# Optimization experiments

Hardware: AMD Instinct MI355X
Metric: run time of the kernel (lower is better)

The kernel has to match this reference:

```python
import jax, jax.numpy as jnp
import numpy as np

N = 50000      # nodes
E = 400000     # edges (before self-loops)
IN = 128
HID = 64
HEADS = 8
OUT = 3
NEG_SLOPE = 0.2
EPS = 1e-6


def setup_inputs() -> dict:
    key = jax.random.key(0)
    ks = jax.random.split(key, 32)
    def nrm(k, shape, s=0.05):
        return jax.random.normal(k, shape, dtype=jnp.float32) * s
    inp = {}
    inp['x'] = nrm(ks[0], (N, IN), 1.0)
    inp['edge_index'] = jax.random.randint(ks[1], (2, E), 0, N)
    inp['res_W'] = nrm(ks[2], (OUT, IN))
    inp['res_b'] = jnp.zeros((OUT,), jnp.float32)
    # (in, out, heads, concat) per GAT layer
    dims = [(IN, HID, HEADS, True), (HID * HEADS, HID, HEADS, True),
            (HID * HEADS, HID, HEADS, True), (HID * HEADS, OUT, 1, False)]
    j = 3
    for i, (ci, co, h, cc) in enumerate(dims):
        inp['ln_g%d' % i] = jnp.ones((ci,), jnp.float32)
        inp['ln_b%d' % i] = jnp.zeros((ci,), jnp.float32)
        inp['W%d' % i] = nrm(ks[j], (h * co, ci)); j += 1
        inp['asr%d' % i] = nrm(ks[j], (h, co)); j += 1
        inp['adt%d' % i] = nrm(ks[j], (h, co)); j += 1
        inp['b%d' % i] = jnp.zeros((h * co if cc else co,), jnp.float32)
    return inp


def layer_norm(x, g, b):
    mu = x.mean(-1, keepdims=True)
    var = ((x - mu) ** 2).mean(-1, keepdims=True)
    return (x - mu) / jnp.sqrt(var + EPS) * g + b


def gat_conv(x, src, dst, W, a_src, a_dst, bias, heads, co, concat):
    n = x.shape[0]
    h = (x @ W.T).reshape(n, heads, co)                    # [N,H,C]
    al_src = jnp.sum(h * a_src, axis=-1)                   # [N,H]
    al_dst = jnp.sum(h * a_dst, axis=-1)                   # [N,H]
    e = jax.nn.leaky_relu(al_src[src] + al_dst[dst], NEG_SLOPE)  # [E',H]
    # segment softmax over incoming edges of each destination node
    m = jax.ops.segment_max(e, dst, num_segments=n)
    e = jnp.exp(e - m[dst])
    s = jax.ops.segment_sum(e, dst, num_segments=n)
    alpha = e / s[dst]                                     # [E',H]
    msg = h[src] * alpha[..., None]                        # [E',H,C]
    out = jax.ops.segment_sum(msg, dst, num_segments=n)    # [N,H,C]
    out = out.reshape(n, heads * co) if concat else out.mean(axis=1)
    return out + bias


def reference(x, edge_index, res_W, res_b,
              ln_g0, ln_b0, W0, asr0, adt0, b0,
              ln_g1, ln_b1, W1, asr1, adt1, b1,
              ln_g2, ln_b2, W2, asr2, adt2, b2,
              ln_g3, ln_b3, W3, asr3, adt3, b3):
    n = x.shape[0]
    loops = jnp.arange(n)
    src = jnp.concatenate([edge_index[0], loops])          # add self-loops (PyG default)
    dst = jnp.concatenate([edge_index[1], loops])
    residual = x @ res_W.T + res_b
    layers = [(ln_g0, ln_b0, W0, asr0, adt0, b0, HEADS, HID, True),
              (ln_g1, ln_b1, W1, asr1, adt1, b1, HEADS, HID, True),
              (ln_g2, ln_b2, W2, asr2, adt2, b2, HEADS, HID, True),
              (ln_g3, ln_b3, W3, asr3, adt3, b3, 1, OUT, False)]
    h = x
    num_layers = len(layers)
    for i, (g, bb, W, a_s, a_d, bi, hd, co, cc) in enumerate(layers):
        x_res = h
        h = layer_norm(h, g, bb)
        h = gat_conv(h, src, dst, W, a_s, a_d, bi, hd, co, cc)
        if i < num_layers - 1:
            h = jax.nn.gelu(h, approximate=False)
            if h.shape == x_res.shape:
                h = h + x_res
    return h + residual
```

## Files before the change

kernel.cpp:

```cpp
#include <hip/hip_runtime.h>
#include <math.h>

#define NN 50000
#define MPAD 50048
#define EE 400000
#define NE 450000
#define IN_F 128
#define NEG_SLOPE 0.2f
#define EPSV 1e-6f

typedef unsigned short bf16u;
typedef short bf8_t __attribute__((ext_vector_type(8)));
typedef float f32x4 __attribute__((ext_vector_type(4)));

__device__ __forceinline__ float bf2f(unsigned int u) {
    return __uint_as_float(u << 16);
}
__device__ __forceinline__ bf16u f2bf(float f) {
    unsigned int u = __float_as_uint(f);
    unsigned int r = (u + 0x7FFFu + ((u >> 16) & 1u)) >> 16;
    return (bf16u)r;
}
__device__ __forceinline__ float gelu_f(float v) {
    return 0.5f * v * (1.0f + erff(v * 0.70710678118654752f));
}

__device__ __forceinline__ void gload_lds16(const void* g, void* l) {
    __builtin_amdgcn_global_load_lds(
        (__attribute__((address_space(1))) void*)(g),
        (__attribute__((address_space(3))) void*)(l), 16, 0, 0);
}

__global__ void k_zero_i32(int* p, int n) {
    int i = blockIdx.x * 256 + threadIdx.x;
    if (i < n) p[i] = 0;
}

__global__ void k_deg(const int* __restrict__ ei, int* __restrict__ deg) {
    int i = blockIdx.x * 256 + threadIdx.x;
    if (i >= NE) return;
    int d = (i < EE) ? ei[EE + i] : (i - EE);
    atomicAdd(&deg[d], 1);
}

__global__ __launch_bounds__(256) void k_scan1(const int* __restrict__ deg,
                                               int* __restrict__ incl,
                                               int* __restrict__ bsums, int n) {
    __shared__ int sm[1024];
    int base = blockIdx.x * 1024;
    for (int i = threadIdx.x; i < 1024; i += 256)
        sm[i] = (base + i < n) ? deg[base + i] : 0;
    __syncthreads();
    for (int off = 1; off < 1024; off <<= 1) {
        int v[4];
#pragma unroll
        for (int j = 0; j < 4; j++) {
            int i = threadIdx.x + 256 * j;
            v[j] = (i >= off) ? sm[i - off] : 0;
        }
        __syncthreads();
#pragma unroll
        for (int j = 0; j < 4; j++) {
            int i = threadIdx.x + 256 * j;
            sm[i] += v[j];
        }
        __syncthreads();
    }
    for (int i = threadIdx.x; i < 1024; i += 256)
        if (base + i < n) incl[base + i] = sm[i];
    if (threadIdx.x == 0) bsums[blockIdx.x] = sm[1023];
}

__global__ void k_scan2(int* bsums, int nb) {
    if (threadIdx.x == 0 && blockIdx.x == 0) {
        int run = 0;
        for (int i = 0; i < nb; i++) { int v = bsums[i]; bsums[i] = run; run += v; }
    }
}

__global__ void k_scan3(const int* __restrict__ deg, int* __restrict__ rowptr,
                        int* __restrict__ cursor, const int* __restrict__ bsums,
                        int n, int ne) {
    int i = blockIdx.x * 256 + threadIdx.x;
    if (i < n) {
        int excl = rowptr[i] + bsums[i >> 10] - deg[i];
        rowptr[i] = excl;
        cursor[i] = excl;
    }
    if (i == n) rowptr[n] = ne;
}

__global__ void k_scatter(const int* __restrict__ ei, int* __restrict__ cursor,
                          int* __restrict__ col) {
    int i = blockIdx.x * 256 + threadIdx.x;
    if (i >= NE) return;
    int s, d;
    if (i < EE) { s = ei[i]; d = ei[EE + i]; }
    else        { s = i - EE; d = i - EE; }
    int p = atomicAdd(&cursor[d], 1);
    col[p] = s;
}

__global__ void k_cast(const float* __restrict__ x, bf16u* __restrict__ h, int total) {
    int i = blockIdx.x * 256 + threadIdx.x;
    if (i < total) h[i] = f2bf(x[i]);
}

__global__ __launch_bounds__(256) void k_castln(const float* __restrict__ x,
                                                bf16u* __restrict__ h,
                                                float* __restrict__ stats, int n) {
    int row = (blockIdx.x * 256 + threadIdx.x) >> 6;
    int lane = threadIdx.x & 63;
    if (row >= n) return;
    float2 v = *(const float2*)(x + (size_t)row * 128 + lane * 2);
    unsigned int pk = (unsigned int)f2bf(v.x) | ((unsigned int)f2bf(v.y) << 16);
    *(unsigned int*)(h + (size_t)row * 128 + lane * 2) = pk;
    float s = v.x + v.y, s2 = v.x * v.x + v.y * v.y;
#pragma unroll
    for (int off = 32; off; off >>= 1) {
        s  += __shfl_xor(s, off);
        s2 += __shfl_xor(s2, off);
    }
    if (lane == 0) {
        float mu = s * (1.0f / 128.0f);
        float var = s2 * (1.0f / 128.0f) - mu * mu;
        stats[row * 2 + 0] = mu;
        stats[row * 2 + 1] = rsqrtf(var + EPSV);
    }
}

__global__ __launch_bounds__(256) void k_residual(const float* __restrict__ x,
                                                  const float* __restrict__ rw,
                                                  const float* __restrict__ rb,
                                                  float* __restrict__ res) {
    int gw = (blockIdx.x * 256 + threadIdx.x) >> 6;
    int lane = threadIdx.x & 63;
    if (gw >= NN) return;
    float a0 = 0.f, a1 = 0.f, a2 = 0.f;
    for (int k = lane; k < IN_F; k += 64) {
        float xv = x[(size_t)gw * IN_F + k];
        a0 += xv * rw[0 * IN_F + k];
        a1 += xv * rw[1 * IN_F + k];
        a2 += xv * rw[2 * IN_F + k];
    }
#pragma unroll
    for (int off = 32; off; off >>= 1) {
        a0 += __shfl_down(a0, off);
        a1 += __shfl_down(a1, off);
        a2 += __shfl_down(a2, off);
    }
    if (lane == 0) {
        res[gw * 3 + 0] = a0 + rb[0];
        res[gw * 3 + 1] = a1 + rb[1];
        res[gw * 3 + 2] = a2 + rb[2];
    }
}

#define BM 128
#define BN 128
#define BKK 32
__global__ __launch_bounds__(256) void k_gemm_mfma(const bf16u* __restrict__ H,
                                                   const float* __restrict__ stats,
                                                   const float* __restrict__ g,
                                                   const float* __restrict__ bbias,
                                                   const bf16u* __restrict__ Wb,
                                                   bf16u* __restrict__ C,
                                                   int Mreal, int ci, int K) {
    __shared__ __align__(16) bf16u As[BM * BKK];
    __shared__ __align__(16) bf16u Bs[BN * BKK];
    const int tid = threadIdx.x;
    const int w = tid >> 6, lane = tid & 63;
    const int row0 = blockIdx.x * BM, col0 = blockIdx.y * BN;
    const int wr = (w >> 1) * 64, wc = (w & 1) * 64;

    const int srow = w * 32 + (lane >> 2);
    const int scol = (lane & 3) * 8;
    const bf16u* gA = H + (size_t)(row0 + srow) * ci + scol;
    const bf16u* gB = Wb + (size_t)(col0 + srow) * ci + scol;
    const float mu1 = stats[(row0 + srow) * 2 + 0];
    const float rs1 = stats[(row0 + srow) * 2 + 1];
    const float mu2 = stats[(row0 + srow + 16) * 2 + 0];
    const float rs2 = stats[(row0 + srow + 16) * 2 + 1];
    bf16u* lA1 = &As[(size_t)srow * BKK + scol];
    bf16u* lA2 = &As[(size_t)(srow + 16) * BKK + scol];
    void* lB1 = &Bs[(size_t)(w * 32) * BKK];
    void* lB2 = &Bs[(size_t)(w * 32 + 16) * BKK];

    f32x4 acc[4][4] = {};

    const int fr = lane & 15;
    const int fk = (lane >> 4) * 8;

    for (int k0 = 0; k0 < ci; k0 += BKK) {
        uint4 ra1 = *(const uint4*)(gA + k0);
        uint4 ra2 = *(const uint4*)(gA + (size_t)16 * ci + k0);
        float4 g0 = *(const float4*)(g + k0 + scol);
        float4 g1 = *(const float4*)(g + k0 + scol + 4);
        float4 b0 = *(const float4*)(bbias + k0 + scol);
        float4 b1 = *(const float4*)(bbias + k0 + scol + 4);
        float gg[8] = {g0.x, g0.y, g0.z, g0.w, g1.x, g1.y, g1.z, g1.w};
        float bb[8] = {b0.x, b0.y, b0.z, b0.w, b1.x, b1.y, b1.z, b1.w};
        unsigned int u1[4] = {ra1.x, ra1.y, ra1.z, ra1.w};
        unsigned int u2[4] = {ra2.x, ra2.y, ra2.z, ra2.w};
        uint4 p1, p2;
        {
            unsigned int po[4], qo[4];
#pragma unroll
            for (int j = 0; j < 4; j++) {
                float va = (bf2f(u1[j] & 0xFFFFu) - mu1) * rs1;
                float vb = (bf2f(u1[j] >> 16)     - mu1) * rs1;
                float oa = fmaf(va, gg[2 * j], bb[2 * j]);
                float ob = fmaf(vb, gg[2 * j + 1], bb[2 * j + 1]);
                po[j] = (unsigned int)f2bf(oa) | ((unsigned int)f2bf(ob) << 16);
                float vc = (bf2f(u2[j] & 0xFFFFu) - mu2) * rs2;
                float vd = (bf2f(u2[j] >> 16)     - mu2) * rs2;
                float oc = fmaf(vc, gg[2 * j], bb[2 * j]);
                float od = fmaf(vd, gg[2 * j + 1], bb[2 * j + 1]);
                qo[j] = (unsigned int)f2bf(oc) | ((unsigned int)f2bf(od) << 16);
            }
            p1 = make_uint4(po[0], po[1], po[2], po[3]);
            p2 = make_uint4(qo[0], qo[1], qo[2], qo[3]);
        }

        __syncthreads();
        *(uint4*)lA1 = p1;
        *(uint4*)lA2 = p2;
        gload_lds16(gB + k0, lB1);
        gload_lds16(gB + (size_t)16 * ci + k0, lB2);
        __syncthreads();

        bf8_t af[4], bf[4];
#pragma unroll
        for (int m = 0; m < 4; m++)
            af[m] = *(const bf8_t*)&As[(size_t)(wr + m * 16 + fr) * BKK + fk];
#pragma unroll
        for (int n = 0; n < 4; n++)
            bf[n] = *(const bf8_t*)&Bs[(size_t)(wc + n * 16 + fr) * BKK + fk];
#pragma unroll
        for (int m = 0; m < 4; m++)
#pragma unroll
            for (int n = 0; n < 4; n++)
                acc[m][n] = __builtin_amdgcn_mfma_f32_16x16x32_bf16(af[m], bf[n], acc[m][n], 0, 0, 0);
    }

    const int fc = lane & 15;
    const int fq = (lane >> 4) * 4;
#pragma unroll
    for (int m = 0; m < 4; m++) {
#pragma unroll
        for (int r = 0; r < 4; r++) {
            int row = row0 + wr + m * 16 + fq + r;
            if (row >= Mreal) continue;
#pragma unroll
            for (int n = 0; n < 4; n++) {
                int col = col0 + wc + n * 16 + fc;
                C[(size_t)row * K + col] = f2bf(acc[m][n][r]);
            }
        }
    }
}

__global__ __launch_bounds__(256) void k_al2(const bf16u* __restrict__ hlin,
                                             const float* __restrict__ asr,
                                             const float* __restrict__ adt,
                                             float* __restrict__ alsrc,
                                             float* __restrict__ aldst, int n) {
    int row = (blockIdx.x * 256 + threadIdx.x) >> 6;
    int lane = threadIdx.x & 63;
    if (row >= n) return;
    int h = lane >> 3, c0 = (lane & 7) * 8;
    uint4 u = *(const uint4*)(hlin + (size_t)row * 512 + lane * 8);
    const float* as = asr + h * 64 + c0;
    const float* ad = adt + h * 64 + c0;
    float4 s0 = *(const float4*)as, s1 = *(const float4*)(as + 4);
    float4 d0 = *(const float4*)ad, d1 = *(const float4*)(ad + 4);
    float v0 = bf2f(u.x & 0xFFFFu), v1 = bf2f(u.x >> 16);
    float v2 = bf2f(u.y & 0xFFFFu), v3 = bf2f(u.y >> 16);
    float v4 = bf2f(u.z & 0xFFFFu), v5 = bf2f(u.z >> 16);
    float v6 = bf2f(u.w & 0xFFFFu), v7 = bf2f(u.w >> 16);
    float ss = v0 * s0.x + v1 * s0.y + v2 * s0.z + v3 * s0.w
             + v4 * s1.x + v5 * s1.y + v6 * s1.z + v7 * s1.w;
    float dd = v0 * d0.x + v1 * d0.y + v2 * d0.z + v3 * d0.w
             + v4 * d1.x + v5 * d1.y + v6 * d1.z + v7 * d1.w;
#pragma unroll
    for (int off = 4; off; off >>= 1) {
        ss += __shfl_xor(ss, off);
        dd += __shfl_xor(dd, off);
    }
    if ((lane & 7) == 0) {
        alsrc[row * 8 + h] = ss;
        aldst[row * 8 + h] = dd;
    }
}

__global__ __launch_bounds__(256) void k_lin3(const bf16u* __restrict__ h,
                                              const float* __restrict__ stats,
                                              const float* __restrict__ g,
                                              const float* __restrict__ bb,
                                              const float* __restrict__ W,
                                              const float* __restrict__ a_s,
                                              const float* __restrict__ a_d,
                                              bf16u* __restrict__ hlin3,
                                              float* __restrict__ alsrc,
                                              float* __restrict__ aldst, int n) {
    int row = (blockIdx.x * 256 + threadIdx.x) >> 6;
    int lane = threadIdx.x & 63;
    if (row >= n) return;
    float mu = stats[row * 2 + 0], rs = stats[row * 2 + 1];
    uint4 r = *(const uint4*)(h + (size_t)row * 512 + lane * 8);
    float4 g0 = *(const float4*)(g + lane * 8);
    float4 g1 = *(const float4*)(g + lane * 8 + 4);
    float4 b0 = *(const float4*)(bb + lane * 8);
    float4 b1 = *(const float4*)(bb + lane * 8 + 4);
    float gg[8] = {g0.x, g0.y, g0.z, g0.w, g1.x, g1.y, g1.z, g1.w};
    float bv[8] = {b0.x, b0.y, b0.z, b0.w, b1.x, b1.y, b1.z, b1.w};
    unsigned int u[4] = {r.x, r.y, r.z, r.w};
    float ln[8];
#pragma unroll
    for (int j = 0; j < 4; j++) {
        ln[2 * j]     = fmaf((bf2f(u[j] & 0xFFFFu) - mu) * rs, gg[2 * j], bv[2 * j]);
        ln[2 * j + 1] = fmaf((bf2f(u[j] >> 16)     - mu) * rs, gg[2 * j + 1], bv[2 * j + 1]);
    }
    float a0 = 0.f, a1 = 0.f, a2 = 0.f;
#pragma unroll
    for (int j = 0; j < 8; j++) {
        int k = lane * 8 + j;
        a0 += ln[j] * W[k];
        a1 += ln[j] * W[512 + k];
        a2 += ln[j] * W[1024 + k];
    }
#pragma unroll
    for (int off = 32; off; off >>= 1) {
        a0 += __shfl_down(a0, off);
        a1 += __shfl_down(a1, off);
        a2 += __shfl_down(a2, off);
    }
    if (lane == 0) {
        hlin3[row * 3 + 0] = f2bf(a0);
        hlin3[row * 3 + 1] = f2bf(a1);
        hlin3[row * 3 + 2] = f2bf(a2);
        alsrc[row] = a0 * a_s[0] + a1 * a_s[1] + a2 * a_s[2];
        aldst[row] = a0 * a_d[0] + a1 * a_d[1] + a2 * a_d[2];
    }
}

__global__ __launch_bounds__(256) void k_aggN(const bf16u* __restrict__ hlin,
                                              const float* __restrict__ alsrc,
                                              const float* __restrict__ aldst,
                                              const int* __restrict__ rowptr,
                                              const int* __restrict__ col,
                                              const float* __restrict__ bias,
                                              bf16u* __restrict__ hio,
                                              float* __restrict__ stats,
                                              int n, int dores) {
    __shared__ float alds[4][8][66];
    int wv = threadIdx.x >> 6;
    int node = (blockIdx.x * 256 + threadIdx.x) >> 6;
    int lane = threadIdx.x & 63;
    if (node >= n) return;
    int beg = rowptr[node], end = rowptr[node + 1];
    int deg = end - beg;

    const float4* dv = (const float4*)(aldst + node * 8);
    float4 da = dv[0], db = dv[1];
    float ad[8] = {da.x, da.y, da.z, da.w, db.x, db.y, db.z, db.w};

    float s = 0.f, s2 = 0.f;

    if (deg <= 64) {
        int srcreg = 0;
        float raw[8];
#pragma unroll
        for (int h = 0; h < 8; h++) raw[h] = -INFINITY;
        if (lane < deg) {
            srcreg = col[beg + lane];
            const float4* sv = (const float4*)(alsrc + srcreg * 8);
            float4 sa = sv[0], sb = sv[1];
            float sl[8] = {sa.x, sa.y, sa.z, sa.w, sb.x, sb.y, sb.z, sb.w};
#pragma unroll
            for (int h = 0; h < 8; h++) {
                float v = sl[h] + ad[h];
                raw[h] = (v >= 0.f) ? v : NEG_SLOPE * v;
            }
        }
        float m[8];
#pragma unroll
        for (int h = 0; h < 8; h++) m[h] = raw[h];
#pragma unroll
        for (int off = 32; off; off >>= 1)
#pragma unroll
            for (int h = 0; h < 8; h++) m[h] = fmaxf(m[h], __shfl_xor(m[h], off));
        float ex[8], sm[8];
#pragma unroll
        for (int h = 0; h < 8; h++) {
            ex[h] = (lane < deg) ? __expf(raw[h] - m[h]) : 0.f;
            sm[h] = ex[h];
        }
#pragma unroll
        for (int off = 32; off; off >>= 1)
#pragma unroll
            for (int h = 0; h < 8; h++) sm[h] += __shfl_xor(sm[h], off);
#pragma unroll
        for (int h = 0; h < 8; h++)
            alds[wv][h][lane] = ex[h] * (1.0f / sm[h]);
        asm volatile("s_waitcnt lgkmcnt(0)" ::: "memory");

        int hl = lane >> 3;
        const float* myal = &alds[wv][hl][0];
        float acc[8] = {};
        for (int e = 0; e < deg; e++) {
            float alpha = myal[e];
            int src = __shfl(srcreg, e);
            uint4 u = *(const uint4*)(hlin + ((size_t)src << 9) + (lane << 3));
            acc[0] = fmaf(alpha, bf2f(u.x & 0xFFFFu), acc[0]);
            acc[1] = fmaf(alpha, bf2f(u.x >> 16),     acc[1]);
            acc[2] = fmaf(alpha, bf2f(u.y & 0xFFFFu), acc[2]);
            acc[3] = fmaf(alpha, bf2f(u.y >> 16),     acc[3]);
            acc[4] = fmaf(alpha, bf2f(u.z & 0xFFFFu), acc[4]);
            acc[5] = fmaf(alpha, bf2f(u.z >> 16),     acc[5]);
            acc[6] = fmaf(alpha, bf2f(u.w & 0xFFFFu), acc[6]);
            acc[7] = fmaf(alpha, bf2f(u.w >> 16),     acc[7]);
        }

        size_t idx = (size_t)node * 512 + lane * 8;
        float4 b0 = *(const float4*)(bias + lane * 8);
        float4 b1 = *(const float4*)(bias + lane * 8 + 4);
        float bb[8] = {b0.x, b0.y, b0.z, b0.w, b1.x, b1.y, b1.z, b1.w};
        float fin[8];
#pragma unroll
        for (int j = 0; j < 8; j++) fin[j] = gelu_f(acc[j] + bb[j]);
        if (dores) {
            uint4 up = *(const uint4*)(hio + idx);
            fin[0] += bf2f(up.x & 0xFFFFu); fin[1] += bf2f(up.x >> 16);
            fin[2] += bf2f(up.y & 0xFFFFu); fin[3] += bf2f(up.y >> 16);
            fin[4] += bf2f(up.z & 0xFFFFu); fin[5] += bf2f(up.z >> 16);
            fin[6] += bf2f(up.w & 0xFFFFu); fin[7] += bf2f(up.w >> 16);
        }
        uint4 pk;
        pk.x = (unsigned int)f2bf(fin[0]) | ((unsigned int)f2bf(fin[1]) << 16);
        pk.y = (unsigned int)f2bf(fin[2]) | ((unsigned int)f2bf(fin[3]) << 16);
        pk.z = (unsigned int)f2bf(fin[4]) | ((unsigned int)f2bf(fin[5]) << 16);
        pk.w = (unsigned int)f2bf(fin[6]) | ((unsigned int)f2bf(fin[7]) << 16);
        *(uint4*)(hio + idx) = pk;
#pragma unroll
        for (int j = 0; j < 8; j++) { s += fin[j]; s2 += fin[j] * fin[j]; }
    } else {
        for (int h = 0; h < 8; h++) {
            float adh = ad[h];
            float m = -INFINITY;
            for (int e = beg + lane; e < end; e += 64) {
                float v = alsrc[col[e] * 8 + h] + adh;
                v = (v >= 0.f) ? v : NEG_SLOPE * v;
                m = fmaxf(m, v);
            }
#pragma unroll
            for (int off = 32; off; off >>= 1) m = fmaxf(m, __shfl_xor(m, off));
            float sum = 0.f;
            for (int e = beg + lane; e < end; e += 64) {
                float v = alsrc[col[e] * 8 + h] + adh;
                v = (v >= 0.f) ? v : NEG_SLOPE * v;
                sum += __expf(v - m);
            }
#pragma unroll
            for (int off = 32; off; off >>= 1) sum += __shfl_xor(sum, off);
            float inv = 1.0f / sum;
            float acc = 0.f;
            for (int e = beg; e < end; e++) {
                int src = col[e];
                float v = alsrc[src * 8 + h] + adh;
                v = (v >= 0.f) ? v : NEG_SLOPE * v;
                float alpha = __expf(v - m) * inv;
                acc = fmaf(alpha, bf2f(hlin[((size_t)src << 9) + h * 64 + lane]), acc);
            }
            float fin = gelu_f(acc + bias[h * 64 + lane]);
            size_t idx = (size_t)node * 512 + h * 64 + lane;
            if (dores) fin += bf2f(hio[idx]);
            hio[idx] = f2bf(fin);
            s += fin; s2 += fin * fin;
        }
    }

#pragma unroll
    for (int off = 32; off; off >>= 1) {
        s  += __shfl_xor(s, off);
        s2 += __shfl_xor(s2, off);
    }
    if (lane == 0) {
        float mu = s * (1.0f / 512.0f);
        float var = s2 * (1.0f / 512.0f) - mu * mu;
        stats[node * 2 + 0] = mu;
        stats[node * 2 + 1] = rsqrtf(var + EPSV);
    }
}

__global__ __launch_bounds__(256) void k_aggF(const bf16u* __restrict__ hlin,
                                              const float* __restrict__ alsrc,
                                              const float* __restrict__ aldst,
                                              const int* __restrict__ rowptr,
                                              const int* __restrict__ col,
                                              const float* __restrict__ bias,
                                              float* __restrict__ outf,
                                              const float* __restrict__ resid, int n) {
    int node = (blockIdx.x * 256 + threadIdx.x) >> 6;
    int lane = threadIdx.x & 63;
    if (node >= n) return;
    int beg = rowptr[node], end = rowptr[node + 1];
    float adh = aldst[node];

    float m = -INFINITY;
    for (int e = beg + lane; e < end; e += 64) {
        float v = alsrc[col[e]] + adh;
        v = (v >= 0.f) ? v : NEG_SLOPE * v;
        m = fmaxf(m, v);
    }
#pragma unroll
    for (int off = 32; off; off >>= 1) m = fmaxf(m, __shfl_xor(m, off));

    float sum = 0.f;
    for (int e = beg + lane; e < end; e += 64) {
        float v = alsrc[col[e]] + adh;
        v = (v >= 0.f) ? v : NEG_SLOPE * v;
        sum += __expf(v - m);
    }
#pragma unroll
    for (int off = 32; off; off >>= 1) sum += __shfl_xor(sum, off);
    float inv = 1.0f / sum;

    float acc = 0.f;
    for (int e = beg; e < end; e++) {
        int src = col[e];
        float v = alsrc[src] + adh;
        v = (v >= 0.f) ? v : NEG_SLOPE * v;
        float alpha = __expf(v - m) * inv;
        if (lane < 3) acc += alpha * bf2f(hlin[(size_t)src * 3 + lane]);
    }
    if (lane < 3)
        outf[node * 3 + lane] = acc + bias[lane] + resid[node * 3 + lane];
}

extern "C" void kernel_launch(void* const* d_in, const int* in_sizes, int n_in,
                              void* d_out, int out_size, void* d_ws, size_t ws_size,
                              hipStream_t stream) {
    const float* x    = (const float*)d_in[0];
    const int*   ei   = (const int*)d_in[1];
    const float* resW = (const float*)d_in[2];
    const float* resb = (const float*)d_in[3];
    const float *lng[4], *lnb[4], *Wm[4], *asr[4], *adt[4], *bias[4];
    int idx = 4;
    for (int i = 0; i < 4; i++) {
        lng[i]  = (const float*)d_in[idx++];
        lnb[i]  = (const float*)d_in[idx++];
        Wm[i]   = (const float*)d_in[idx++];
        asr[i]  = (const float*)d_in[idx++];
        adt[i]  = (const float*)d_in[idx++];
        bias[i] = (const float*)d_in[idx++];
    }

    char* base = (char*)d_ws;
    size_t off = 0;
    auto alloc = [&](size_t bytes) {
        void* p = base + off;
        off += (bytes + 255) & ~(size_t)255;
        return p;
    };
    bf16u* hbuf  = (bf16u*)alloc((size_t)MPAD * 512 * 2);
    bf16u* lbuf  = (bf16u*)alloc((size_t)MPAD * 512 * 2);
    bf16u* wb0   = (bf16u*)alloc((size_t)512 * 128 * 2);
    bf16u* wb1   = (bf16u*)alloc((size_t)512 * 512 * 2);
    bf16u* wb2   = (bf16u*)alloc((size_t)512 * 512 * 2);
    float* stats = (float*)alloc((size_t)MPAD * 2 * 4);
    float* alsrc = (float*)alloc((size_t)NN * 8 * 4);
    float* aldst = (float*)alloc((size_t)NN * 8 * 4);
    float* resid = (float*)alloc((size_t)NN * 3 * 4);
    int* rowptr  = (int*)alloc((size_t)(NN + 1) * 4);
    int* cursor  = (int*)alloc((size_t)NN * 4);
    int* deg     = (int*)alloc((size_t)NN * 4);
    int* colidx  = (int*)alloc((size_t)NE * 4);
    int* bsums   = (int*)alloc(256 * 4);
    if (off > ws_size) return;

    float* out = (float*)d_out;

    k_zero_i32<<<(NN + 255) / 256, 256, 0, stream>>>(deg, NN);
    k_deg<<<(NE + 255) / 256, 256, 0, stream>>>(ei, deg);
    int nb = (NN + 1023) / 1024;
    k_scan1<<<nb, 256, 0, stream>>>(deg, rowptr, bsums, NN);
    k_scan2<<<1, 64, 0, stream>>>(bsums, nb);
    k_scan3<<<(NN + 1 + 255) / 256, 256, 0, stream>>>(deg, rowptr, cursor, bsums, NN, NE);
    k_scatter<<<(NE + 255) / 256, 256, 0, stream>>>(ei, cursor, colidx);

    int rowBlocks = (NN * 64 + 255) / 256;
    k_residual<<<rowBlocks, 256, 0, stream>>>(x, resW, resb, resid);
    k_castln<<<rowBlocks, 256, 0, stream>>>(x, hbuf, stats, NN);
    k_cast<<<(512 * 128 + 255) / 256, 256, 0, stream>>>(Wm[0], wb0, 512 * 128);
    k_cast<<<(512 * 512 + 255) / 256, 256, 0, stream>>>(Wm[1], wb1, 512 * 512);
    k_cast<<<(512 * 512 + 255) / 256, 256, 0, stream>>>(Wm[2], wb2, 512 * 512);

    const bf16u* wb[3] = {wb0, wb1, wb2};
    const int ci_a[3] = {128, 512, 512};

    for (int i = 0; i < 3; i++) {
        int ci = ci_a[i];
        int dores = (i >= 1) ? 1 : 0;

        dim3 ggrid(MPAD / BM, 512 / BN);
        k_gemm_mfma<<<ggrid, 256, 0, stream>>>(hbuf, stats, lng[i], lnb[i], wb[i],
                                               lbuf, NN, ci, 512);

        k_al2<<<rowBlocks, 256, 0, stream>>>(lbuf, asr[i], adt[i], alsrc, aldst, NN);

        k_aggN<<<rowBlocks, 256, 0, stream>>>(lbuf, alsrc, aldst, rowptr, colidx,
                                              bias[i], hbuf, stats, NN, dores);
    }

    k_lin3<<<rowBlocks, 256, 0, stream>>>(hbuf, stats, lng[3], lnb[3], Wm[3],
                                          asr[3], adt[3], lbuf, alsrc, aldst, NN);
    k_aggF<<<rowBlocks, 256, 0, stream>>>(lbuf, alsrc, aldst, rowptr, colidx,
                                          bias[3], out, resid, NN);
}
```

Measured before the change: 704.5 us.

## Fuse attention logits into GEMM epilogue, merge residual into cast, rework aggregation

Computes the per-head attention logits (alsrc/aldst) in the MFMA GEMM epilogue from fp32 accumulators. This removes the separate k_al2 pass that re-read the bf16 projection. The residual projection is merged into the cast/LayerNorm-stats kernel, so x is read once. The aggregation kernel stores precomputed byte offsets next to alpha in LDS and unrolls the gather by two. The final layer uses a padded 4-wide hlin3 layout with a single-pass warp softmax for low-degree nodes. Logits now come from unrounded fp32 values instead of bf16, which slightly changes numerics, and the epilogue adds shuffle reductions.

New measurement: 670.1 us. 4.9% less time.

```diff
diff --git a/kernel.cpp b/kernel.cpp
--- a/kernel.cpp
+++ b/kernel.cpp
@@ -15,6 +15,9 @@
 
 __device__ __forceinline__ float bf2f(unsigned int u) {
     return __uint_as_float(u << 16);
+}
+__device__ __forceinline__ float bf2f_hi(unsigned int u) {
+    return __uint_as_float(u & 0xFFFF0000u);
 }
 __device__ __forceinline__ bf16u f2bf(float f) {
     unsigned int u = __float_as_uint(f);
@@ -106,53 +109,41 @@
     if (i < total) h[i] = f2bf(x[i]);
 }
 
-__global__ __launch_bounds__(256) void k_castln(const float* __restrict__ x,
-                                                bf16u* __restrict__ h,
-                                                float* __restrict__ stats, int n) {
+__global__ __launch_bounds__(256) void k_castres(const float* __restrict__ x,
+                                                 const float* __restrict__ rw,
+                                                 const float* __restrict__ rb,
+                                                 bf16u* __restrict__ h,
+                                                 float* __restrict__ stats,
+                                                 float* __restrict__ res, int n) {
     int row = (blockIdx.x * 256 + threadIdx.x) >> 6;
     int lane = threadIdx.x & 63;
     if (row >= n) return;
     float2 v = *(const float2*)(x + (size_t)row * 128 + lane * 2);
     unsigned int pk = (unsigned int)f2bf(v.x) | ((unsigned int)f2bf(v.y) << 16);
     *(unsigned int*)(h + (size_t)row * 128 + lane * 2) = pk;
+    float2 w0 = *(const float2*)(rw + 0 * 128 + lane * 2);
+    float2 w1 = *(const float2*)(rw + 1 * 128 + lane * 2);
+    float2 w2 = *(const float2*)(rw + 2 * 128 + lane * 2);
     float s = v.x + v.y, s2 = v.x * v.x + v.y * v.y;
+    float a0 = v.x * w0.x + v.y * w0.y;
+    float a1 = v.x * w1.x + v.y * w1.y;
+    float a2 = v.x * w2.x + v.y * w2.y;
 #pragma unroll
     for (int off = 32; off; off >>= 1) {
         s  += __shfl_xor(s, off);
         s2 += __shfl_xor(s2, off);
+        a0 += __shfl_xor(a0, off);
+        a1 += __shfl_xor(a1, off);
+        a2 += __shfl_xor(a2, off);
     }
     if (lane == 0) {
         float mu = s * (1.0f / 128.0f);
         float var = s2 * (1.0f / 128.0f) - mu * mu;
         stats[row * 2 + 0] = mu;
         stats[row * 2 + 1] = rsqrtf(var + EPSV);
-    }
-}
-
-__global__ __launch_bounds__(256) void k_residual(const float* __restrict__ x,
-                                                  const float* __restrict__ rw,
-                                                  const float* __restrict__ rb,
-                                                  float* __restrict__ res) {
-    int gw = (blockIdx.x * 256 + threadIdx.x) >> 6;
-    int lane = threadIdx.x & 63;
-    if (gw >= NN) return;
-    float a0 = 0.f, a1 = 0.f, a2 = 0.f;
-    for (int k = lane; k < IN_F; k += 64) {
-        float xv = x[(size_t)gw * IN_F + k];
-        a0 += xv * rw[0 * IN_F + k];
-        a1 += xv * rw[1 * IN_F + k];
-        a2 += xv * rw[2 * IN_F + k];
-    }
-#pragma unroll
-    for (int off = 32; off; off >>= 1) {
-        a0 += __shfl_down(a0, off);
-        a1 += __shfl_down(a1, off);
-        a2 += __shfl_down(a2, off);
-    }
-    if (lane == 0) {
-        res[gw * 3 + 0] = a0 + rb[0];
-        res[gw * 3 + 1] = a1 + rb[1];
-        res[gw * 3 + 2] = a2 + rb[2];
+        res[row * 3 + 0] = a0 + rb[0];
+        res[row * 3 + 1] = a1 + rb[1];
+        res[row * 3 + 2] = a2 + rb[2];
     }
 }
 
@@ -165,6 +156,10 @@
                                                    const float* __restrict__ bbias,
                                                    const bf16u* __restrict__ Wb,
                                                    bf16u* __restrict__ C,
+                                                   const float* __restrict__ asr,
+                                                   const float* __restrict__ adt,
+                                                   float* __restrict__ alsrc,
+                                                   float* __restrict__ aldst,
                                                    int Mreal, int ci, int K) {
     __shared__ __align__(16) bf16u As[BM * BKK];
     __shared__ __align__(16) bf16u Bs[BN * BKK];
@@ -208,12 +203,12 @@
 #pragma unroll
             for (int j = 0; j < 4; j++) {
                 float va = (bf2f(u1[j] & 0xFFFFu) - mu1) * rs1;
-                float vb = (bf2f(u1[j] >> 16)     - mu1) * rs1;
+                float vb = (bf2f_hi(u1[j])         - mu1) * rs1;
                 float oa = fmaf(va, gg[2 * j], bb[2 * j]);
                 float ob = fmaf(vb, gg[2 * j + 1], bb[2 * j + 1]);
                 po[j] = (unsigned int)f2bf(oa) | ((unsigned int)f2bf(ob) << 16);
                 float vc = (bf2f(u2[j] & 0xFFFFu) - mu2) * rs2;
-                float vd = (bf2f(u2[j] >> 16)     - mu2) * rs2;
+                float vd = (bf2f_hi(u2[j])         - mu2) * rs2;
                 float oc = fmaf(vc, gg[2 * j], bb[2 * j]);
                 float od = fmaf(vd, gg[2 * j + 1], bb[2 * j + 1]);
                 qo[j] = (unsigned int)f2bf(oc) | ((unsigned int)f2bf(od) << 16);
@@ -245,6 +240,7 @@
 
     const int fc = lane & 15;
     const int fq = (lane >> 4) * 4;
+
 #pragma unroll
     for (int m = 0; m < 4; m++) {
 #pragma unroll
@@ -258,38 +254,33 @@
             }
         }
     }
-}
-
-__global__ __launch_bounds__(256) void k_al2(const bf16u* __restrict__ hlin,
-                                             const float* __restrict__ asr,
-                                             const float* __restrict__ adt,
-                                             float* __restrict__ alsrc,
-                                             float* __restrict__ aldst, int n) {
-    int row = (blockIdx.x * 256 + threadIdx.x) >> 6;
-    int lane = threadIdx.x & 63;
-    if (row >= n) return;
-    int h = lane >> 3, c0 = (lane & 7) * 8;
-    uint4 u = *(const uint4*)(hlin + (size_t)row * 512 + lane * 8);
-    const float* as = asr + h * 64 + c0;
-    const float* ad = adt + h * 64 + c0;
-    float4 s0 = *(const float4*)as, s1 = *(const float4*)(as + 4);
-    float4 d0 = *(const float4*)ad, d1 = *(const float4*)(ad + 4);
-    float v0 = bf2f(u.x & 0xFFFFu), v1 = bf2f(u.x >> 16);
-    float v2 = bf2f(u.y & 0xFFFFu), v3 = bf2f(u.y >> 16);
-    float v4 = bf2f(u.z & 0xFFFFu), v5 = bf2f(u.z >> 16);
-    float v6 = bf2f(u.w & 0xFFFFu), v7 = bf2f(u.w >> 16);
-    float ss = v0 * s0.x + v1 * s0.y + v2 * s0.z + v3 * s0.w
-             + v4 * s1.x + v5 * s1.y + v6 * s1.z + v7 * s1.w;
-    float dd = v0 * d0.x + v1 * d0.y + v2 * d0.z + v3 * d0.w
-             + v4 * d1.x + v5 * d1.y + v6 * d1.z + v7 * d1.w;
-#pragma unroll
-    for (int off = 4; off; off >>= 1) {
-        ss += __shfl_xor(ss, off);
-        dd += __shfl_xor(dd, off);
-    }
-    if ((lane & 7) == 0) {
-        alsrc[row * 8 + h] = ss;
-        aldst[row * 8 + h] = dd;
+
+    const int head = blockIdx.y * 2 + (wc >> 6);
+    float av[4], dv[4];
+#pragma unroll
+    for (int n = 0; n < 4; n++) {
+        av[n] = asr[head * 64 + n * 16 + fc];
+        dv[n] = adt[head * 64 + n * 16 + fc];
+    }
+#pragma unroll
+    for (int m = 0; m < 4; m++) {
+#pragma unroll
+        for (int r = 0; r < 4; r++) {
+            float s1 = acc[m][0][r] * av[0] + acc[m][1][r] * av[1]
+                     + acc[m][2][r] * av[2] + acc[m][3][r] * av[3];
+            float s2 = acc[m][0][r] * dv[0] + acc[m][1][r] * dv[1]
+                     + acc[m][2][r] * dv[2] + acc[m][3][r] * dv[3];
+#pragma unroll
+            for (int o = 1; o < 16; o <<= 1) {
+                s1 += __shfl_xor(s1, o);
+                s2 += __shfl_xor(s2, o);
+            }
+            int row = row0 + wr + m * 16 + fq + r;
+            if (fc == 0 && row < Mreal) {
+                alsrc[row * 8 + head] = s1;
+                aldst[row * 8 + head] = s2;
+            }
+        }
     }
 }
 
@@ -319,7 +310,7 @@
 #pragma unroll
     for (int j = 0; j < 4; j++) {
         ln[2 * j]     = fmaf((bf2f(u[j] & 0xFFFFu) - mu) * rs, gg[2 * j], bv[2 * j]);
-        ln[2 * j + 1] = fmaf((bf2f(u[j] >> 16)     - mu) * rs, gg[2 * j + 1], bv[2 * j + 1]);
+        ln[2 * j + 1] = fmaf((bf2f_hi(u[j])         - mu) * rs, gg[2 * j + 1], bv[2 * j + 1]);
     }
     float a0 = 0.f, a1 = 0.f, a2 = 0.f;
 #pragma unroll
@@ -336,9 +327,9 @@
         a2 += __shfl_down(a2, off);
     }
     if (lane == 0) {
-        hlin3[row * 3 + 0] = f2bf(a0);
-        hlin3[row * 3 + 1] = f2bf(a1);
-        hlin3[row * 3 + 2] = f2bf(a2);
+        *(unsigned int*)(hlin3 + (size_t)row * 4) =
+            (unsigned int)f2bf(a0) | ((unsigned int)f2bf(a1) << 16);
+        *(unsigned int*)(hlin3 + (size_t)row * 4 + 2) = (unsigned int)f2bf(a2);
         alsrc[row] = a0 * a_s[0] + a1 * a_s[1] + a2 * a_s[2];
         aldst[row] = a0 * a_d[0] + a1 * a_d[1] + a2 * a_d[2];
     }
@@ -353,7 +344,7 @@
                                               bf16u* __restrict__ hio,
                                               float* __restrict__ stats,
                                               int n, int dores) {
-    __shared__ float alds[4][8][66];
+    __shared__ uint2 aldsU[4][8][66];
     int wv = threadIdx.x >> 6;
     int node = (blockIdx.x * 256 + threadIdx.x) >> 6;
     int lane = threadIdx.x & 63;
@@ -361,19 +352,20 @@
     int beg = rowptr[node], end = rowptr[node + 1];
     int deg = end - beg;
 
-    const float4* dv = (const float4*)(aldst + node * 8);
-    float4 da = dv[0], db = dv[1];
+    const float4* dvv = (const float4*)(aldst + node * 8);
+    float4 da = dvv[0], db = dvv[1];
     float ad[8] = {da.x, da.y, da.z, da.w, db.x, db.y, db.z, db.w};
 
     float s = 0.f, s2 = 0.f;
 
     if (deg <= 64) {
-        int srcreg = 0;
+        unsigned int offb = 0;
         float raw[8];
 #pragma unroll
         for (int h = 0; h < 8; h++) raw[h] = -INFINITY;
         if (lane < deg) {
-            srcreg = col[beg + lane];
+            int srcreg = col[beg + lane];
+            offb = (unsigned int)srcreg << 10;
             const float4* sv = (const float4*)(alsrc + srcreg * 8);
             float4 sa = sv[0], sb = sv[1];
             float sl[8] = {sa.x, sa.y, sa.z, sa.w, sb.x, sb.y, sb.z, sb.w};
@@ -401,25 +393,54 @@
 #pragma unroll
             for (int h = 0; h < 8; h++) sm[h] += __shfl_xor(sm[h], off);
 #pragma unroll
-        for (int h = 0; h < 8; h++)
-            alds[wv][h][lane] = ex[h] * (1.0f / sm[h]);
+        for (int h = 0; h < 8; h++) {
+            uint2 t;
+            t.x = __float_as_uint(ex[h] * (1.0f / sm[h]));
+            t.y = offb;
+            aldsU[wv][h][lane] = t;
+        }
         asm volatile("s_waitcnt lgkmcnt(0)" ::: "memory");
 
         int hl = lane >> 3;
-        const float* myal = &alds[wv][hl][0];
+        const uint2* myal = &aldsU[wv][hl][0];
+        const char* base2 = (const char*)hlin + (lane << 4);
         float acc[8] = {};
-        for (int e = 0; e < deg; e++) {
-            float alpha = myal[e];
-            int src = __shfl(srcreg, e);
-            uint4 u = *(const uint4*)(hlin + ((size_t)src << 9) + (lane << 3));
-            acc[0] = fmaf(alpha, bf2f(u.x & 0xFFFFu), acc[0]);
-            acc[1] = fmaf(alpha, bf2f(u.x >> 16),     acc[1]);
-            acc[2] = fmaf(alpha, bf2f(u.y & 0xFFFFu), acc[2]);
-            acc[3] = fmaf(alpha, bf2f(u.y >> 16),     acc[3]);
-            acc[4] = fmaf(alpha, bf2f(u.z & 0xFFFFu), acc[4]);
-            acc[5] = fmaf(alpha, bf2f(u.z >> 16),     acc[5]);
-            acc[6] = fmaf(alpha, bf2f(u.w & 0xFFFFu), acc[6]);
-            acc[7] = fmaf(alpha, bf2f(u.w >> 16),     acc[7]);
+        int e = 0;
+        for (; e + 2 <= deg; e += 2) {
+            uint2 t0 = myal[e];
+            uint2 t1 = myal[e + 1];
+            uint4 u0 = *(const uint4*)(base2 + t0.y);
+            uint4 u1 = *(const uint4*)(base2 + t1.y);
+            float a0 = __uint_as_float(t0.x), a1 = __uint_as_float(t1.x);
+            acc[0] = fmaf(a0, bf2f(u0.x & 0xFFFFu), acc[0]);
+            acc[1] = fmaf(a0, bf2f_hi(u0.x),        acc[1]);
+            acc[2] = fmaf(a0, bf2f(u0.y & 0xFFFFu), acc[2]);
+            acc[3] = fmaf(a0, bf2f_hi(u0.y),        acc[3]);
+            acc[4] = fmaf(a0, bf2f(u0.z & 0xFFFFu), acc[4]);
+            acc[5] = fmaf(a0, bf2f_hi(u0.z),        acc[5]);
+            acc[6] = fmaf(a0, bf2f(u0.w & 0xFFFFu), acc[6]);
+            acc[7] = fmaf(a0, bf2f_hi(u0.w),        acc[7]);
+            acc[0] = fmaf(a1, bf2f(u1.x & 0xFFFFu), acc[0]);
+            acc[1] = fmaf(a1, bf2f_hi(u1.x),        acc[1]);
+            acc[2] = fmaf(a1, bf2f(u1.y & 0xFFFFu), acc[2]);
+            acc[3] = fmaf(a1, bf2f_hi(u1.y),        acc[3]);
+            acc[4] = fmaf(a1, bf2f(u1.z & 0xFFFFu), acc[4]);
+            acc[5] = fmaf(a1, bf2f_hi(u1.z),        acc[5]);
+            acc[6] = fmaf(a1, bf2f(u1.w & 0xFFFFu), acc[6]);
+            acc[7] = fmaf(a1, bf2f_hi(u1.w),        acc[7]);
+        }
+        if (e < deg) {
+            uint2 t0 = myal[e];
+            uint4 u0 = *(const uint4*)(base2 + t0.y);
+            float a0 = __uint_as_float(t0.x);
+            acc[0] = fmaf(a0, bf2f(u0.x & 0xFFFFu), acc[0]);
+            acc[1] = fmaf(a0, bf2f_hi(u0.x),        acc[1]);
+            acc[2] = fmaf(a0, bf2f(u0.y & 0xFFFFu), acc[2]);
+            acc[3] = fmaf(a0, bf2f_hi(u0.y),        acc[3]);
+            acc[4] = fmaf(a0, bf2f(u0.z & 0xFFFFu), acc[4]);
+            acc[5] = fmaf(a0, bf2f_hi(u0.z),        acc[5]);
+            acc[6] = fmaf(a0, bf2f(u0.w & 0xFFFFu), acc[6]);
+            acc[7] = fmaf(a0, bf2f_hi(u0.w),        acc[7]);
         }
 
         size_t idx = (size_t)node * 512 + lane * 8;
@@ -431,10 +452,10 @@
         for (int j = 0; j < 8; j++) fin[j] = gelu_f(acc[j] + bb[j]);
         if (dores) {
             uint4 up = *(const uint4*)(hio + idx);
-            fin[0] += bf2f(up.x & 0xFFFFu); fin[1] += bf2f(up.x >> 16);
-            fin[2] += bf2f(up.y & 0xFFFFu); fin[3] += bf2f(up.y >> 16);
-            fin[4] += bf2f(up.z & 0xFFFFu); fin[5] += bf2f(up.z >> 16);
-            fin[6] += bf2f(up.w & 0xFFFFu); fin[7] += bf2f(up.w >> 16);
+            fin[0] += bf2f(up.x & 0xFFFFu); fin[1] += bf2f_hi(up.x);
+            fin[2] += bf2f(up.y & 0xFFFFu); fin[3] += bf2f_hi(up.y);
+            fin[4] += bf2f(up.z & 0xFFFFu); fin[5] += bf2f_hi(up.z);
+            fin[6] += bf2f(up.w & 0xFFFFu); fin[7] += bf2f_hi(up.w);
         }
         uint4 pk;
         pk.x = (unsigned int)f2bf(fin[0]) | ((unsigned int)f2bf(fin[1]) << 16);
@@ -493,7 +514,7 @@
     }
 }
 
-__global__ __launch_bounds__(256) void k_aggF(const bf16u* __restrict__ hlin,
+__global__ __launch_bounds__(256) void k_aggF(const bf16u* __restrict__ hlin3,
                                               const float* __restrict__ alsrc,
                                               const float* __restrict__ aldst,
                                               const int* __restrict__ rowptr,
@@ -505,37 +526,73 @@
     int lane = threadIdx.x & 63;
     if (node >= n) return;
     int beg = rowptr[node], end = rowptr[node + 1];
+    int deg = end - beg;
     float adh = aldst[node];
 
-    float m = -INFINITY;
-    for (int e = beg + lane; e < end; e += 64) {
-        float v = alsrc[col[e]] + adh;
-        v = (v >= 0.f) ? v : NEG_SLOPE * v;
-        m = fmaxf(m, v);
-    }
-#pragma unroll
-    for (int off = 32; off; off >>= 1) m = fmaxf(m, __shfl_xor(m, off));
-
-    float sum = 0.f;
-    for (int e = beg + lane; e < end; e += 64) {
-        float v = alsrc[col[e]] + adh;
-        v = (v >= 0.f) ? v : NEG_SLOPE * v;
-        sum += __expf(v - m);
-    }
-#pragma unroll
-    for (int off = 32; off; off >>= 1) sum += __shfl_xor(sum, off);
-    float inv = 1.0f / sum;
-
-    float acc = 0.f;
-    for (int e = beg; e < end; e++) {
-        int src = col[e];
-        float v = alsrc[src] + adh;
-        v = (v >= 0.f) ? v : NEG_SLOPE * v;
-        float alpha = __expf(v - m) * inv;
-        if (lane < 3) acc += alpha * bf2f(hlin[(size_t)src * 3 + lane]);
-    }
-    if (lane < 3)
-        outf[node * 3 + lane] = acc + bias[lane] + resid[node * 3 + lane];
+    if (deg <= 64) {
+        int src = 0;
+        float raw = -INFINITY;
+        if (lane < deg) {
+            src = col[beg + lane];
+            float v = alsrc[src] + adh;
+            raw = (v >= 0.f) ? v : NEG_SLOPE * v;
+        }
+        float m = raw;
+#pragma unroll
+        for (int off = 32; off; off >>= 1) m = fmaxf(m, __shfl_xor(m, off));
+        float ex = (lane < deg) ? __expf(raw - m) : 0.f;
+        float sum = ex;
+#pragma unroll
+        for (int off = 32; off; off >>= 1) sum += __shfl_xor(sum, off);
+        float alpha = ex / sum;
+
+        float c0 = 0.f, c1 = 0.f, c2 = 0.f;
+        if (lane < deg) {
+            uint2 u = *(const uint2*)(hlin3 + (size_t)src * 4);
+            c0 = alpha * bf2f(u.x & 0xFFFFu);
+            c1 = alpha * bf2f_hi(u.x);
+            c2 = alpha * bf2f(u.y & 0xFFFFu);
+        }
+#pragma unroll
+        for (int off = 32; off; off >>= 1) {
+            c0 += __shfl_xor(c0, off);
+            c1 += __shfl_xor(c1, off);
+            c2 += __shfl_xor(c2, off);
+        }
+        if (lane == 0) {
+            outf[node * 3 + 0] = c0 + bias[0] + resid[node * 3 + 0];
+            outf[node * 3 + 1] = c1 + bias[1] + resid[node * 3 + 1];
+            outf[node * 3 + 2] = c2 + bias[2] + resid[node * 3 + 2];
+        }
+    } else {
+        float m = -INFINITY;
+        for (int e = beg + lane; e < end; e += 64) {
+            float v = alsrc[col[e]] + adh;
+            v = (v >= 0.f) ? v : NEG_SLOPE * v;
+            m = fmaxf(m, v);
+        }
+#pragma unroll
+        for (int off = 32; off; off >>= 1) m = fmaxf(m, __shfl_xor(m, off));
+        float sum = 0.f;
+        for (int e = beg + lane; e < end; e += 64) {
+            float v = alsrc[col[e]] + adh;
+            v = (v >= 0.f) ? v : NEG_SLOPE * v;
+            sum += __expf(v - m);
+        }
+#pragma unroll
+        for (int off = 32; off; off >>= 1) sum += __shfl_xor(sum, off);
+        float inv = 1.0f / sum;
+        float acc = 0.f;
+        for (int e = beg; e < end; e++) {
+            int src = col[e];
+            float v = alsrc[src] + adh;
+            v = (v >= 0.f) ? v : NEG_SLOPE * v;
+            float alpha = __expf(v - m) * inv;
+            if (lane < 3) acc += alpha * bf2f(hlin3[(size_t)src * 4 + lane]);
+        }
+        if (lane < 3)
+            outf[node * 3 + lane] = acc + bias[lane] + resid[node * 3 + lane];
+    }
 }
 
 extern "C" void kernel_launch(void* const* d_in, const int* in_sizes, int n_in,
@@ -590,8 +647,7 @@
     k_scatter<<<(NE + 255) / 256, 256, 0, stream>>>(ei, cursor, colidx);
 
     int rowBlocks = (NN * 64 + 255) / 256;
-    k_residual<<<rowBlocks, 256, 0, stream>>>(x, resW, resb, resid);
-    k_castln<<<rowBlocks, 256, 0, stream>>>(x, hbuf, stats, NN);
+    k_castres<<<rowBlocks, 256, 0, stream>>>(x, resW, resb, hbuf, stats, resid, NN);
     k_cast<<<(512 * 128 + 255) / 256, 256, 0, stream>>>(Wm[0], wb0, 512 * 128);
     k_cast<<<(512 * 512 + 255) / 256, 256, 0, stream>>>(Wm[1], wb1, 512 * 512);
     k_cast<<<(512 * 512 + 255) / 256, 256, 0, stream>>>(Wm[2], wb2, 512 * 512);
@@ -605,9 +661,8 @@
 
         dim3 ggrid(MPAD / BM, 512 / BN);
         k_gemm_mfma<<<ggrid, 256, 0, stream>>>(hbuf, stats, lng[i], lnb[i], wb[i],
-                                               lbuf, NN, ci, 512);
-
-        k_al2<<<rowBlocks, 256, 0, stream>>>(lbuf, asr[i], adt[i], alsrc, aldst, NN);
+                                               lbuf, asr[i], adt[i], alsrc, aldst,
+                                               NN, ci, 512);
 
         k_aggN<<<rowBlocks, 256, 0, stream>>>(lbuf, alsrc, aldst, rowptr, colidx,
                                               bias[i], hbuf, stats, NN, dores);
```
